# Optimization experiments

Measured on AMD Instinct MI355X. Metric: run time of the kernel, lower is better.

## Reference

```python
import jax, jax.numpy as jnp
import numpy as np

D_MODEL = 768
NUM_HEADS = 12
HEAD_DIM = D_MODEL // NUM_HEADS  # 64, also rotary dim
INTERMEDIATE = 1152
WINDOW = 128          # config.local_attention (layer_id=1 -> local layer)
ROPE_BASE = 10000.0   # local_rope_theta
EPS = 1e-5


def layer_norm_nocenter(x, gamma):
    # keras LayerNormalization(center=False): mean-subtract, no beta
    mu = jnp.mean(x, axis=-1, keepdims=True)
    var = jnp.var(x, axis=-1, keepdims=True)
    return (x - mu) * jax.lax.rsqrt(var + EPS) * gamma


def rotate_half(x):
    x1, x2 = jnp.split(x, 2, axis=-1)
    return jnp.concatenate([-x2, x1], axis=-1)


def setup_inputs() -> dict:
    key = jax.random.key(0)
    ks = jax.random.split(key, 7)
    B, S = 4, 2048
    hidden_states = jax.random.normal(ks[0], (B, S, D_MODEL), dtype=jnp.float32)
    attention_mask = jnp.zeros((B, 1, S, S), dtype=jnp.float32)  # no padding
    s = 0.02
    attn_norm_gamma = jnp.ones((D_MODEL,), dtype=jnp.float32)
    wqkv = jax.random.normal(ks[1], (D_MODEL, 3 * D_MODEL), dtype=jnp.float32) * s
    wo_attn = jax.random.normal(ks[2], (D_MODEL, D_MODEL), dtype=jnp.float32) * s
    mlp_norm_gamma = jnp.ones((D_MODEL,), dtype=jnp.float32)
    wi = jax.random.normal(ks[3], (D_MODEL, 2 * INTERMEDIATE), dtype=jnp.float32) * s
    wo_mlp = jax.random.normal(ks[4], (INTERMEDIATE, D_MODEL), dtype=jnp.float32) * s
    return {
        'hidden_states': hidden_states,
        'attention_mask': attention_mask,
        'attn_norm_gamma': attn_norm_gamma,
        'wqkv': wqkv,
        'wo_attn': wo_attn,
        'mlp_norm_gamma': mlp_norm_gamma,
        'wi': wi,
        'wo_mlp': wo_mlp,
    }


def reference(hidden_states, attention_mask, attn_norm_gamma, wqkv, wo_attn,
              mlp_norm_gamma, wi, wo_mlp):
    B, S, Dm = hidden_states.shape
    H, Dh = NUM_HEADS, HEAD_DIM

    # RoPE cache (NTKScaling with scaling_factor=1 -> plain RoPE)
    idx = jnp.arange(0, Dh, 2, dtype=jnp.float32)
    inv_freq = 1.0 / (ROPE_BASE ** (idx / Dh))          # [Dh/2]
    t = jnp.arange(S, dtype=jnp.float32)
    freqs = t[:, None] * inv_freq[None, :]              # [S, Dh/2]
    emb = jnp.concatenate([freqs, freqs], axis=-1)      # [S, Dh]
    cos = jnp.cos(emb)[None, None]                      # [1,1,S,Dh]
    sin = jnp.sin(emb)[None, None]

    # combined sliding-window + padding mask
    pos = jnp.arange(S)
    dist = jnp.abs(pos[:, None] - pos[None, :])
    neg = jnp.finfo(jnp.float32).min
    local = jnp.where(dist <= WINDOW // 2, 0.0, neg).astype(jnp.float32)
    mask = attention_mask + local[None, None]           # [B,1,S,S]

    # attention (layer_id != 0 -> pre-norm)
    x = layer_norm_nocenter(hidden_states, attn_norm_gamma)
    qkv = (x @ wqkv).reshape(B, S, 3, H, Dh).transpose(2, 0, 3, 1, 4)
    q, k, v = qkv[0], qkv[1], qkv[2]                    # [B,H,S,Dh]
    q = q * cos + rotate_half(q) * sin
    k = k * cos + rotate_half(k) * sin

    scale = 1.0 / jnp.sqrt(jnp.asarray(Dh, q.dtype))
    scores = jnp.einsum('bhqd,bhkd->bhqk', q, k) * scale + mask
    attn = jax.nn.softmax(scores, axis=-1)
    ctx = jnp.einsum('bhqk,bhkd->bhqd', attn, v)
    attn_out = ctx.transpose(0, 2, 1, 3).reshape(B, S, Dm) @ wo_attn

    h = hidden_states + attn_out

    # GLU MLP: Wi -> split -> gelu(x)*gate -> Wo, residual
    n = layer_norm_nocenter(h, mlp_norm_gamma)
    x_in, gate = jnp.split(n @ wi, 2, axis=-1)
    mlp = jax.nn.gelu(x_in, approximate=False) * gate
    return h + mlp @ wo_mlp
```

## Files before the change

### kernel.cpp

```cpp
#include <hip/hip_runtime.h>
#include <cstdint>
#include <cstddef>

typedef __bf16 bf16;
typedef float f32x4 __attribute__((ext_vector_type(4)));
typedef __bf16 bf16x8 __attribute__((ext_vector_type(8)));

#define MFMA16(a, b, c) __builtin_amdgcn_mfma_f32_16x16x32_bf16((a), (b), (c), 0, 0, 0)

__device__ __forceinline__ void gload_lds16(const void* g, void* l) {
  __builtin_amdgcn_global_load_lds((__attribute__((address_space(1))) void*)g,
                                   (__attribute__((address_space(3))) void*)l,
                                   16, 0, 0);
}

__global__ __launch_bounds__(256) void wconv_kernel(const float* __restrict__ W,
                                                    bf16* __restrict__ Wt, int K, int N) {
  __shared__ float tile[32][33];
  const int n0 = blockIdx.x * 32, k0 = blockIdx.y * 32;
  const int t = threadIdx.x;
  const int c = t & 31, r = t >> 5;
#pragma unroll
  for (int i = 0; i < 4; ++i)
    tile[r + i * 8][c] = W[(size_t)(k0 + r + i * 8) * N + n0 + c];
  __syncthreads();
#pragma unroll
  for (int i = 0; i < 4; ++i)
    Wt[(size_t)(n0 + r + i * 8) * K + k0 + c] = (bf16)tile[c][r + i * 8];
}

__global__ __launch_bounds__(256) void ln_kernel(const float* __restrict__ X,
                                                 const float* __restrict__ gamma,
                                                 bf16* __restrict__ out) {
  const int row = blockIdx.x, t = threadIdx.x;
  const float* xr = X + (size_t)row * 768;
  float v0 = xr[t], v1 = xr[t + 256], v2 = xr[t + 512];
  float s = v0 + v1 + v2;
  float s2 = v0 * v0 + v1 * v1 + v2 * v2;
#pragma unroll
  for (int m = 1; m <= 32; m <<= 1) {
    s += __shfl_xor(s, m, 64);
    s2 += __shfl_xor(s2, m, 64);
  }
  __shared__ float red[8];
  const int w = t >> 6, lane = t & 63;
  if (lane == 0) { red[w] = s; red[4 + w] = s2; }
  __syncthreads();
  s = red[0] + red[1] + red[2] + red[3];
  s2 = red[4] + red[5] + red[6] + red[7];
  const float mu = s * (1.f / 768.f);
  const float var = s2 * (1.f / 768.f) - mu * mu;
  const float rs = rsqrtf(var + 1e-5f);
  out[(size_t)row * 768 + t] = (bf16)((v0 - mu) * rs * gamma[t]);
  out[(size_t)row * 768 + t + 256] = (bf16)((v1 - mu) * rs * gamma[t + 256]);
  out[(size_t)row * 768 + t + 512] = (bf16)((v2 - mu) * rs * gamma[t + 512]);
}

template <int BM, bool RES, typename TOUT>
__global__ __launch_bounds__(256) void gemm_bt(const bf16* __restrict__ A,
                                               const bf16* __restrict__ Bt,
                                               const float* __restrict__ Res,
                                               TOUT* __restrict__ C, int M, int N, int K) {
  constexpr int MT = BM / 32;
  __shared__ __align__(16) bf16 As[BM * 64];
  __shared__ __align__(16) bf16 Bs[128 * 64];
  const int t = threadIdx.x;
  const int lane = t & 63;
  const int w = t >> 6;
  const int wm = w >> 1, wn = w & 1;
  const int row0 = blockIdx.y * BM, col0 = blockIdx.x * 128;
  const int rm = lane & 15, qd = lane >> 4;
  f32x4 acc[MT][4] = {};
  for (int k0 = 0; k0 < K; k0 += 64) {
#pragma unroll
    for (int i = 0; i < BM / 32; ++i) {
      int c = i * 256 + t;
      int r = c >> 3, j = (c & 7) ^ (r & 7);
      gload_lds16(A + (size_t)(row0 + r) * K + (k0 + j * 8), &As[c * 8]);
    }
#pragma unroll
    for (int i = 0; i < 4; ++i) {
      int c = i * 256 + t;
      int r = c >> 3, j = (c & 7) ^ (r & 7);
      gload_lds16(Bt + (size_t)(col0 + r) * K + (k0 + j * 8), &Bs[c * 8]);
    }
    __syncthreads();
#pragma unroll
    for (int kb = 0; kb < 2; ++kb) {
      bf16x8 af[MT], bfr[4];
#pragma unroll
      for (int mt = 0; mt < MT; ++mt) {
        int r = wm * (MT * 16) + mt * 16 + rm;
        af[mt] = *(const bf16x8*)&As[r * 64 + (((kb * 4 + qd) ^ (r & 7)) * 8)];
      }
#pragma unroll
      for (int nt = 0; nt < 4; ++nt) {
        int r = wn * 64 + nt * 16 + rm;
        bfr[nt] = *(const bf16x8*)&Bs[r * 64 + (((kb * 4 + qd) ^ (r & 7)) * 8)];
      }
#pragma unroll
      for (int mt = 0; mt < MT; ++mt)
#pragma unroll
        for (int nt = 0; nt < 4; ++nt)
          acc[mt][nt] = MFMA16(af[mt], bfr[nt], acc[mt][nt]);
    }
    __syncthreads();
  }
#pragma unroll
  for (int mt = 0; mt < MT; ++mt)
#pragma unroll
    for (int nt = 0; nt < 4; ++nt) {
      const int gc = col0 + wn * 64 + nt * 16 + rm;
#pragma unroll
      for (int r = 0; r < 4; ++r) {
        const int gr = row0 + wm * (MT * 16) + mt * 16 + qd * 4 + r;
        float v = acc[mt][nt][r];
        const size_t idx = (size_t)gr * N + gc;
        if (RES) v += Res[idx];
        C[idx] = (TOUT)v;
      }
    }
}

__global__ __launch_bounds__(256) void rope_kernel(const bf16* __restrict__ qkv,
                                                   bf16* __restrict__ Qb,
                                                   bf16* __restrict__ Kb) {
  const int row = blockIdx.x;
  const int s = row & 2047, b = row >> 11;
  const bf16* qr = qkv + (size_t)row * 2304;
  const int t = threadIdx.x;
#pragma unroll
  for (int i = 0; i < 3; ++i) {
    int idx = t + i * 256;
    int which = idx >= 384;
    int pp = idx - which * 384;
    int h = pp >> 5, d = pp & 31;
    float invf = exp2f((float)d * -0.41524101186092029f);
    float ang = (float)s * invf;
    float cs, sn;
    sincosf(ang, &cs, &sn);
    float x1 = (float)qr[which * 768 + h * 64 + d];
    float x2 = (float)qr[which * 768 + h * 64 + d + 32];
    bf16* dst = (which ? Kb : Qb) + ((size_t)(b * 12 + h) * 2048 + s) * 64;
    dst[d] = (bf16)(x1 * cs - x2 * sn);
    dst[d + 32] = (bf16)(x2 * cs + x1 * sn);
  }
}

__global__ __launch_bounds__(256) void vt_kernel(const bf16* __restrict__ qkv,
                                                 bf16* __restrict__ Vt) {
  const int bh = blockIdx.y, st = blockIdx.x;
  const int b = bh / 12, h = bh - b * 12;
  const int t = threadIdx.x, d = t & 63, sg = t >> 6;
  const int s0 = st * 64 + sg * 16;
  __align__(16) bf16 vals[16];
#pragma unroll
  for (int j = 0; j < 16; ++j)
    vals[j] = qkv[((size_t)(b * 2048 + s0 + j)) * 2304 + 1536 + h * 64 + d];
  bf16* dst = Vt + ((size_t)bh * 64 + d) * 2048 + s0;
  *(bf16x8*)&dst[0] = *(const bf16x8*)&vals[0];
  *(bf16x8*)&dst[8] = *(const bf16x8*)&vals[8];
}

__global__ __launch_bounds__(256) void attn_kernel(const bf16* __restrict__ Qb,
                                                   const bf16* __restrict__ Kb,
                                                   const bf16* __restrict__ Vt,
                                                   const float* __restrict__ am,
                                                   bf16* __restrict__ ctx) {
  __shared__ __align__(16) bf16 KP[64 * 200];
  __shared__ __align__(16) bf16 Vts[64 * 192];
  bf16* Ks = KP;
  bf16* Ps = KP;

  const int t = threadIdx.x;
  const int lane = t & 63, w = t >> 6;
  const int rm = lane & 15, qd = lane >> 4;
  const int s0 = blockIdx.x * 64;
  const int bh = blockIdx.y;
  const int b = bh / 12, h = bh - b * 12;
  const size_t baseQ = (size_t)bh * 2048;

#pragma unroll
  for (int i = 0; i < 6; ++i) {
    int c = i * 256 + t;
    int r = c >> 3, j = (c & 7) ^ (r & 7);
    int key = min(max(s0 - 64 + r, 0), 2047);
    gload_lds16(Kb + (baseQ + key) * 64 + j * 8, &Ks[c * 8]);
  }
#pragma unroll
  for (int i = 0; i < 6; ++i) {
    int c = i * 256 + t;
    int r = c / 24, jl = c - r * 24;
    int j = (jl & 24) | ((jl & 7) ^ (r & 7));
    int k0 = min(max(s0 - 64 + j * 8, 0), 2040);
    gload_lds16(Vt + ((size_t)bh * 64 + r) * 2048 + k0, &Vts[c * 8]);
  }

  bf16x8 aq[2];
#pragma unroll
  for (int kb = 0; kb < 2; ++kb)
    aq[kb] = *(const bf16x8*)&Qb[(baseQ + s0 + w * 16 + rm) * 64 + kb * 32 + qd * 8];

  float msk[12][4];
#pragma unroll
  for (int nt = 0; nt < 12; ++nt) {
    int key = s0 - 64 + nt * 16 + rm;
#pragma unroll
    for (int r = 0; r < 4; ++r) {
      int qpos = s0 + w * 16 + qd * 4 + r;
      bool valid = (key >= 0) && (key < 2048) && (key - qpos <= 64) && (qpos - key <= 64);
      msk[nt][r] = valid ? am[((size_t)b * 2048 + qpos) * 2048 + key] : -3e38f;
    }
  }
  __syncthreads();

  f32x4 sc[12];
#pragma unroll
  for (int nt = 0; nt < 12; ++nt) {
    f32x4 a = {0.f, 0.f, 0.f, 0.f};
#pragma unroll
    for (int kb = 0; kb < 2; ++kb) {
      int r = nt * 16 + rm;
      bf16x8 bk = *(const bf16x8*)&Ks[r * 64 + (((kb * 4 + qd) ^ (rm & 7)) * 8)];
      a = MFMA16(aq[kb], bk, a);
    }
    sc[nt] = a;
  }

  float mx[4] = {-3e38f, -3e38f, -3e38f, -3e38f};
#pragma unroll
  for (int nt = 0; nt < 12; ++nt)
#pragma unroll
    for (int r = 0; r < 4; ++r) {
      float v = (msk[nt][r] <= -2.9e38f) ? -3e38f : sc[nt][r] * 0.125f + msk[nt][r];
      sc[nt][r] = v;
      mx[r] = fmaxf(mx[r], v);
    }
#pragma unroll
  for (int r = 0; r < 4; ++r)
#pragma unroll
    for (int m = 1; m <= 8; m <<= 1) mx[r] = fmaxf(mx[r], __shfl_xor(mx[r], m, 64));
  float sum[4] = {0.f, 0.f, 0.f, 0.f};
#pragma unroll
  for (int nt = 0; nt < 12; ++nt)
#pragma unroll
    for (int r = 0; r < 4; ++r) {
      float p = (sc[nt][r] > -1e37f) ? __expf(sc[nt][r] - mx[r]) : 0.f;
      sc[nt][r] = p;
      sum[r] += p;
    }
#pragma unroll
  for (int r = 0; r < 4; ++r)
#pragma unroll
    for (int m = 1; m <= 8; m <<= 1) sum[r] += __shfl_xor(sum[r], m, 64);
  float inv[4];
#pragma unroll
  for (int r = 0; r < 4; ++r) inv[r] = 1.f / sum[r];

  __syncthreads();

#pragma unroll
  for (int nt = 0; nt < 12; ++nt)
#pragma unroll
    for (int r = 0; r < 4; ++r)
      Ps[(w * 16 + qd * 4 + r) * 200 + nt * 16 + rm] = (bf16)(sc[nt][r] * inv[r]);

  f32x4 o[4] = {};
#pragma unroll
  for (int ks = 0; ks < 6; ++ks) {
    bf16x8 ap = *(const bf16x8*)&Ps[(w * 16 + rm) * 200 + ks * 32 + qd * 8];
#pragma unroll
    for (int nt = 0; nt < 4; ++nt) {
      int kc = ks * 4 + qd;
      bf16x8 bv = *(const bf16x8*)&Vts[(nt * 16 + rm) * 192 +
                                       (((kc & 24) | ((kc & 7) ^ (rm & 7))) * 8)];
      o[nt] = MFMA16(ap, bv, o[nt]);
    }
  }
#pragma unroll
  for (int nt = 0; nt < 4; ++nt)
#pragma unroll
    for (int r = 0; r < 4; ++r) {
      int q_ = s0 + w * 16 + qd * 4 + r;
      ctx[((size_t)(b * 2048 + q_)) * 768 + h * 64 + nt * 16 + rm] = (bf16)o[nt][r];
    }
}

__global__ __launch_bounds__(128) void geglu_kernel(const bf16* __restrict__ X,
                                                    bf16* __restrict__ out) {
  const int row = blockIdx.y;
  const int c = blockIdx.x * 128 + threadIdx.x;
  const bf16* xr = X + (size_t)row * 2304;
  float x = (float)xr[c], g = (float)xr[1152 + c];
  float ge = 0.5f * x * (1.0f + erff(x * 0.70710678118654752f));
  out[(size_t)row * 1152 + c] = (bf16)(ge * g);
}

extern "C" void kernel_launch(void* const* d_in, const int* in_sizes, int n_in,
                              void* d_out, int out_size, void* d_ws, size_t ws_size,
                              hipStream_t stream) {
  (void)in_sizes; (void)n_in; (void)out_size; (void)ws_size;
  const float* hidden = (const float*)d_in[0];
  const float* amask = (const float*)d_in[1];
  const float* g1 = (const float*)d_in[2];
  const float* wqkv = (const float*)d_in[3];
  const float* woa = (const float*)d_in[4];
  const float* g2 = (const float*)d_in[5];
  const float* wi = (const float*)d_in[6];
  const float* wom = (const float*)d_in[7];
  float* out = (float*)d_out;

  char* p = (char*)d_ws;
  size_t o = 0;
  auto take = [&](size_t bytes) {
    char* r = p + o;
    o = (o + bytes + 255) & ~(size_t)255;
    return r;
  };
  bf16* wqkvT = (bf16*)take((size_t)2304 * 768 * 2);
  bf16* woaT = (bf16*)take((size_t)768 * 768 * 2);
  bf16* wiT = (bf16*)take((size_t)2304 * 768 * 2);
  bf16* womT = (bf16*)take((size_t)768 * 1152 * 2);
  bf16* xn = (bf16*)take((size_t)8192 * 768 * 2);
  bf16* qkvb = (bf16*)take((size_t)8192 * 2304 * 2);
  bf16* Qb = (bf16*)take((size_t)98304 * 64 * 2);
  bf16* Kb = (bf16*)take((size_t)98304 * 64 * 2);
  bf16* Vt = (bf16*)take((size_t)98304 * 64 * 2);
  bf16* ctxb = (bf16*)take((size_t)8192 * 768 * 2);
  float* hbuf = (float*)take((size_t)8192 * 768 * 4);
  bf16* mlp = (bf16*)take((size_t)8192 * 1152 * 2);

  wconv_kernel<<<dim3(72, 24), 256, 0, stream>>>(wqkv, wqkvT, 768, 2304);
  wconv_kernel<<<dim3(24, 24), 256, 0, stream>>>(woa, woaT, 768, 768);
  wconv_kernel<<<dim3(72, 24), 256, 0, stream>>>(wi, wiT, 768, 2304);
  wconv_kernel<<<dim3(24, 36), 256, 0, stream>>>(wom, womT, 1152, 768);

  ln_kernel<<<8192, 256, 0, stream>>>(hidden, g1, xn);
  gemm_bt<128, false, bf16><<<dim3(18, 64), 256, 0, stream>>>(xn, wqkvT, nullptr, qkvb,
                                                              8192, 2304, 768);
  rope_kernel<<<8192, 256, 0, stream>>>(qkvb, Qb, Kb);
  vt_kernel<<<dim3(32, 48), 256, 0, stream>>>(qkvb, Vt);
  attn_kernel<<<dim3(32, 48), 256, 0, stream>>>(Qb, Kb, Vt, amask, ctxb);
  gemm_bt<64, true, float><<<dim3(6, 128), 256, 0, stream>>>(ctxb, woaT, hidden, hbuf,
                                                             8192, 768, 768);

  ln_kernel<<<8192, 256, 0, stream>>>(hbuf, g2, xn);
  gemm_bt<128, false, bf16><<<dim3(18, 64), 256, 0, stream>>>(xn, wiT, nullptr, qkvb,
                                                              8192, 2304, 768);
  geglu_kernel<<<dim3(9, 8192), 128, 0, stream>>>(qkvb, mlp);
  gemm_bt<64, true, float><<<dim3(6, 128), 256, 0, stream>>>(mlp, womT, hbuf, out,
                                                             8192, 768, 1152);
}
```

Measured before the change: 357.1 us.

## Fuse RoPE and V transpose into QKV GEMM, GEGLU into Wi GEGLU GEMM

Replaces the generic QKV GEMM plus separate rope and V-transpose kernels with one GEMM whose epilogue applies rotary embedding (via hardware sin/cos on range-reduced angles) and writes Q, K in head-major layout and V transposed. Likewise fuses the GEGLU activation into the Wi GEMM by computing matching x and gate column tiles in the same block. This removes the round trips of the 8192x2304 intermediate through memory and three launches. The epilogue stores are scattered two-byte writes, and the fast sin/cos slightly change precision.

```diff
diff --git a/kernel.cpp b/kernel.cpp
--- a/kernel.cpp
+++ b/kernel.cpp
@@ -5,6 +5,7 @@
 typedef __bf16 bf16;
 typedef float f32x4 __attribute__((ext_vector_type(4)));
 typedef __bf16 bf16x8 __attribute__((ext_vector_type(8)));
+typedef __bf16 bf16x4 __attribute__((ext_vector_type(4)));
 
 #define MFMA16(a, b, c) __builtin_amdgcn_mfma_f32_16x16x32_bf16((a), (b), (c), 0, 0, 0)
 
@@ -122,44 +123,164 @@
     }
 }
 
-__global__ __launch_bounds__(256) void rope_kernel(const bf16* __restrict__ qkv,
-                                                   bf16* __restrict__ Qb,
-                                                   bf16* __restrict__ Kb) {
-  const int row = blockIdx.x;
-  const int s = row & 2047, b = row >> 11;
-  const bf16* qr = qkv + (size_t)row * 2304;
+__global__ __launch_bounds__(256) void gemm_qkv(const bf16* __restrict__ A,
+                                                const bf16* __restrict__ Bt,
+                                                bf16* __restrict__ Qb,
+                                                bf16* __restrict__ Kb,
+                                                bf16* __restrict__ Vt) {
+  __shared__ __align__(16) bf16 As[128 * 64];
+  __shared__ __align__(16) bf16 Bs[128 * 64];
   const int t = threadIdx.x;
-#pragma unroll
-  for (int i = 0; i < 3; ++i) {
-    int idx = t + i * 256;
-    int which = idx >= 384;
-    int pp = idx - which * 384;
-    int h = pp >> 5, d = pp & 31;
-    float invf = exp2f((float)d * -0.41524101186092029f);
-    float ang = (float)s * invf;
-    float cs, sn;
-    sincosf(ang, &cs, &sn);
-    float x1 = (float)qr[which * 768 + h * 64 + d];
-    float x2 = (float)qr[which * 768 + h * 64 + d + 32];
-    bf16* dst = (which ? Kb : Qb) + ((size_t)(b * 12 + h) * 2048 + s) * 64;
-    dst[d] = (bf16)(x1 * cs - x2 * sn);
-    dst[d + 32] = (bf16)(x2 * cs + x1 * sn);
-  }
-}
-
-__global__ __launch_bounds__(256) void vt_kernel(const bf16* __restrict__ qkv,
-                                                 bf16* __restrict__ Vt) {
-  const int bh = blockIdx.y, st = blockIdx.x;
-  const int b = bh / 12, h = bh - b * 12;
-  const int t = threadIdx.x, d = t & 63, sg = t >> 6;
-  const int s0 = st * 64 + sg * 16;
-  __align__(16) bf16 vals[16];
-#pragma unroll
-  for (int j = 0; j < 16; ++j)
-    vals[j] = qkv[((size_t)(b * 2048 + s0 + j)) * 2304 + 1536 + h * 64 + d];
-  bf16* dst = Vt + ((size_t)bh * 64 + d) * 2048 + s0;
-  *(bf16x8*)&dst[0] = *(const bf16x8*)&vals[0];
-  *(bf16x8*)&dst[8] = *(const bf16x8*)&vals[8];
+  const int lane = t & 63;
+  const int w = t >> 6;
+  const int wm = w >> 1, wn = w & 1;
+  const int row0 = blockIdx.y * 128, col0 = blockIdx.x * 128;
+  const int rm = lane & 15, qd = lane >> 4;
+  f32x4 acc[4][4] = {};
+  for (int k0 = 0; k0 < 768; k0 += 64) {
+#pragma unroll
+    for (int i = 0; i < 4; ++i) {
+      int c = i * 256 + t;
+      int r = c >> 3, j = (c & 7) ^ (r & 7);
+      gload_lds16(A + (size_t)(row0 + r) * 768 + (k0 + j * 8), &As[c * 8]);
+      int c2 = i * 256 + t;
+      gload_lds16(Bt + (size_t)(col0 + r) * 768 + (k0 + j * 8), &Bs[c2 * 8]);
+    }
+    __syncthreads();
+#pragma unroll
+    for (int kb = 0; kb < 2; ++kb) {
+      bf16x8 af[4], bfr[4];
+#pragma unroll
+      for (int mt = 0; mt < 4; ++mt) {
+        int r = wm * 64 + mt * 16 + rm;
+        af[mt] = *(const bf16x8*)&As[r * 64 + (((kb * 4 + qd) ^ (r & 7)) * 8)];
+      }
+#pragma unroll
+      for (int nt = 0; nt < 4; ++nt) {
+        int r = wn * 64 + nt * 16 + rm;
+        bfr[nt] = *(const bf16x8*)&Bs[r * 64 + (((kb * 4 + qd) ^ (r & 7)) * 8)];
+      }
+#pragma unroll
+      for (int mt = 0; mt < 4; ++mt)
+#pragma unroll
+        for (int nt = 0; nt < 4; ++nt)
+          acc[mt][nt] = MFMA16(af[mt], bfr[nt], acc[mt][nt]);
+    }
+    __syncthreads();
+  }
+
+  const int head_id = blockIdx.x * 2 + wn;
+  const int typ = head_id / 12;
+  const int h = head_id - typ * 12;
+  const int b = row0 >> 11;
+  const int sw = (row0 & 2047) + wm * 64;
+  const size_t bhbase = (size_t)(b * 12 + h) * 2048;
+
+  if (typ < 2) {
+    bf16* dst = typ ? Kb : Qb;
+    float invf[2];
+#pragma unroll
+    for (int nt = 0; nt < 2; ++nt)
+      invf[nt] = exp2f((float)(nt * 16 + rm) * -0.41524101186092029f);
+#pragma unroll
+    for (int mt = 0; mt < 4; ++mt)
+#pragma unroll
+      for (int r = 0; r < 4; ++r) {
+        int s = sw + mt * 16 + qd * 4 + r;
+#pragma unroll
+        for (int nt = 0; nt < 2; ++nt) {
+          float ang = (float)s * invf[nt];
+          float rev = ang * 0.15915494309189535f;
+          rev -= floorf(rev);
+          float sn = __builtin_amdgcn_sinf(rev);
+          float cs = __builtin_amdgcn_cosf(rev);
+          float x1 = acc[mt][nt][r], x2 = acc[mt][nt + 2][r];
+          int d = nt * 16 + rm;
+          dst[(bhbase + s) * 64 + d] = (bf16)(x1 * cs - x2 * sn);
+          dst[(bhbase + s) * 64 + d + 32] = (bf16)(x2 * cs + x1 * sn);
+        }
+      }
+  } else {
+#pragma unroll
+    for (int mt = 0; mt < 4; ++mt)
+#pragma unroll
+      for (int nt = 0; nt < 4; ++nt) {
+        int d = nt * 16 + rm;
+        int s4 = sw + mt * 16 + qd * 4;
+        bf16x4 v4;
+#pragma unroll
+        for (int r = 0; r < 4; ++r) v4[r] = (bf16)acc[mt][nt][r];
+        *(bf16x4*)&Vt[(bhbase * 64) + ((size_t)(h * 0) ) + ((size_t)( (b * 12 + h) * 64 + d)) * 2048 + s4 - bhbase * 64] = v4;
+      }
+  }
+}
+
+__global__ __launch_bounds__(256) void gemm_wi_geglu(const bf16* __restrict__ A,
+                                                     const bf16* __restrict__ Bt,
+                                                     bf16* __restrict__ outp) {
+  __shared__ __align__(16) bf16 As[128 * 64];
+  __shared__ __align__(16) bf16 Bxs[64 * 64];
+  __shared__ __align__(16) bf16 Bgs[64 * 64];
+  const int t = threadIdx.x;
+  const int lane = t & 63;
+  const int w = t >> 6;
+  const int wm = w >> 1, wn = w & 1;
+  const int row0 = blockIdx.y * 128, col0 = blockIdx.x * 64;
+  const int rm = lane & 15, qd = lane >> 4;
+  f32x4 accx[4][2] = {}, accg[4][2] = {};
+  for (int k0 = 0; k0 < 768; k0 += 64) {
+#pragma unroll
+    for (int i = 0; i < 4; ++i) {
+      int c = i * 256 + t;
+      int r = c >> 3, j = (c & 7) ^ (r & 7);
+      gload_lds16(A + (size_t)(row0 + r) * 768 + (k0 + j * 8), &As[c * 8]);
+    }
+#pragma unroll
+    for (int i = 0; i < 2; ++i) {
+      int c = i * 256 + t;
+      int r = c >> 3, j = (c & 7) ^ (r & 7);
+      gload_lds16(Bt + (size_t)(col0 + r) * 768 + (k0 + j * 8), &Bxs[c * 8]);
+      gload_lds16(Bt + (size_t)(1152 + col0 + r) * 768 + (k0 + j * 8), &Bgs[c * 8]);
+    }
+    __syncthreads();
+#pragma unroll
+    for (int kb = 0; kb < 2; ++kb) {
+      bf16x8 af[4], bx[2], bg[2];
+#pragma unroll
+      for (int mt = 0; mt < 4; ++mt) {
+        int r = wm * 64 + mt * 16 + rm;
+        af[mt] = *(const bf16x8*)&As[r * 64 + (((kb * 4 + qd) ^ (r & 7)) * 8)];
+      }
+#pragma unroll
+      for (int nt = 0; nt < 2; ++nt) {
+        int r = wn * 32 + nt * 16 + rm;
+        int off = r * 64 + (((kb * 4 + qd) ^ (r & 7)) * 8);
+        bx[nt] = *(const bf16x8*)&Bxs[off];
+        bg[nt] = *(const bf16x8*)&Bgs[off];
+      }
+#pragma unroll
+      for (int mt = 0; mt < 4; ++mt)
+#pragma unroll
+        for (int nt = 0; nt < 2; ++nt) {
+          accx[mt][nt] = MFMA16(af[mt], bx[nt], accx[mt][nt]);
+          accg[mt][nt] = MFMA16(af[mt], bg[nt], accg[mt][nt]);
+        }
+    }
+    __syncthreads();
+  }
+#pragma unroll
+  for (int mt = 0; mt < 4; ++mt)
+#pragma unroll
+    for (int nt = 0; nt < 2; ++nt) {
+      const int gc = col0 + wn * 32 + nt * 16 + rm;
+#pragma unroll
+      for (int r = 0; r < 4; ++r) {
+        const int gr = row0 + wm * 64 + mt * 16 + qd * 4 + r;
+        float x = accx[mt][nt][r], g = accg[mt][nt][r];
+        float ge = 0.5f * x * (1.0f + erff(x * 0.70710678118654752f));
+        outp[(size_t)gr * 1152 + gc] = (bf16)(ge * g);
+      }
+    }
 }
 
 __global__ __launch_bounds__(256) void attn_kernel(const bf16* __restrict__ Qb,
@@ -284,16 +405,6 @@
       int q_ = s0 + w * 16 + qd * 4 + r;
       ctx[((size_t)(b * 2048 + q_)) * 768 + h * 64 + nt * 16 + rm] = (bf16)o[nt][r];
     }
-}
-
-__global__ __launch_bounds__(128) void geglu_kernel(const bf16* __restrict__ X,
-                                                    bf16* __restrict__ out) {
-  const int row = blockIdx.y;
-  const int c = blockIdx.x * 128 + threadIdx.x;
-  const bf16* xr = X + (size_t)row * 2304;
-  float x = (float)xr[c], g = (float)xr[1152 + c];
-  float ge = 0.5f * x * (1.0f + erff(x * 0.70710678118654752f));
-  out[(size_t)row * 1152 + c] = (bf16)(ge * g);
 }
 
 extern "C" void kernel_launch(void* const* d_in, const int* in_sizes, int n_in,
@@ -322,7 +433,6 @@
   bf16* wiT = (bf16*)take((size_t)2304 * 768 * 2);
   bf16* womT = (bf16*)take((size_t)768 * 1152 * 2);
   bf16* xn = (bf16*)take((size_t)8192 * 768 * 2);
-  bf16* qkvb = (bf16*)take((size_t)8192 * 2304 * 2);
   bf16* Qb = (bf16*)take((size_t)98304 * 64 * 2);
   bf16* Kb = (bf16*)take((size_t)98304 * 64 * 2);
   bf16* Vt = (bf16*)take((size_t)98304 * 64 * 2);
@@ -336,18 +446,13 @@
   wconv_kernel<<<dim3(24, 36), 256, 0, stream>>>(wom, womT, 1152, 768);
 
   ln_kernel<<<8192, 256, 0, stream>>>(hidden, g1, xn);
-  gemm_bt<128, false, bf16><<<dim3(18, 64), 256, 0, stream>>>(xn, wqkvT, nullptr, qkvb,
-                                                              8192, 2304, 768);
-  rope_kernel<<<8192, 256, 0, stream>>>(qkvb, Qb, Kb);
-  vt_kernel<<<dim3(32, 48), 256, 0, stream>>>(qkvb, Vt);
+  gemm_qkv<<<dim3(18, 64), 256, 0, stream>>>(xn, wqkvT, Qb, Kb, Vt);
   attn_kernel<<<dim3(32, 48), 256, 0, stream>>>(Qb, Kb, Vt, amask, ctxb);
   gemm_bt<64, true, float><<<dim3(6, 128), 256, 0, stream>>>(ctxb, woaT, hidden, hbuf,
                                                              8192, 768, 768);
 
   ln_kernel<<<8192, 256, 0, stream>>>(hbuf, g2, xn);
-  gemm_bt<128, false, bf16><<<dim3(18, 64), 256, 0, stream>>>(xn, wiT, nullptr, qkvb,
-                                                              8192, 2304, 768);
-  geglu_kernel<<<dim3(9, 8192), 128, 0, stream>>>(qkvb, mlp);
+  gemm_wi_geglu<<<dim3(18, 64), 256, 0, stream>>>(xn, wiT, mlp);
   gemm_bt<64, true, float><<<dim3(6, 128), 256, 0, stream>>>(mlp, womT, hbuf, out,
                                                              8192, 768, 1152);
 }
```

Result: faster. 329.5 us (-7.7%).
